# Performance work log

Measured on AMD Instinct MI355X. Metric: run time of the kernel, lower is better.

The kernel has to match this reference:

```python
import jax, jax.numpy as jnp
import numpy as np

ATTN_MASK_VALUE = -1e10
N, D_IN, D_HEAD, D_OUT = 8192, 1024, 128, 1024


def setup_inputs() -> dict:
    key = jax.random.key(0)
    k_x, k_wqkv, k_bqkv, k_wo, k_bo = jax.random.split(key, 5)
    x = jax.random.normal(k_x, (N, D_IN), dtype=jnp.float32)
    # flax Dense default: lecun_normal kernel, zeros bias; use scaled normal for test
    w_qkv = jax.random.normal(k_wqkv, (D_IN, 3 * D_HEAD), dtype=jnp.float32) / np.sqrt(D_IN)
    b_qkv = jnp.zeros((3 * D_HEAD,), dtype=jnp.float32)
    w_out = jax.random.normal(k_wo, (D_HEAD, D_OUT), dtype=jnp.float32) / np.sqrt(D_HEAD)
    b_out = jnp.zeros((D_OUT,), dtype=jnp.float32)
    return {"x": x, "w_qkv": w_qkv, "b_qkv": b_qkv, "w_out": w_out, "b_out": b_out}


def reference(x, w_qkv, b_qkv, w_out, b_out):
    n = x.shape[0]
    scale = D_HEAD ** (-0.5)
    qkv = x @ w_qkv + b_qkv                      # [n, 3*dh]
    q, k, v = jnp.split(qkv, 3, axis=-1)         # each [n, dh]
    sim = jnp.einsum('id,jd->ij', q, k) * scale  # [n, n]
    mask = jnp.triu(jnp.ones((n, n), dtype=bool), 1)
    sim = jnp.where(mask, ATTN_MASK_VALUE, sim)
    attn = jax.nn.softmax(sim, axis=-1)
    out = jnp.einsum('ij,jd->id', attn, v)       # [n, dh]
    return out @ w_out + b_out                   # [n, d_out]
```

## Files before the change

### kernel.cpp

```cpp
#include <hip/hip_runtime.h>
#include <stdint.h>

typedef __attribute__((ext_vector_type(4))) float f32x4;
typedef __attribute__((ext_vector_type(8))) __bf16 bf16x8;

#define MFMA16(a, b, c) __builtin_amdgcn_mfma_f32_16x16x32_bf16(a, b, c, 0, 0, 0)
#define GLOAD16(g, l)                                                              \
  __builtin_amdgcn_global_load_lds(                                                \
      (const __attribute__((address_space(1))) unsigned int*)(g),                  \
      (__attribute__((address_space(3))) unsigned int*)(l), 16, 0, 0)
#define EXP2F(x) __builtin_amdgcn_exp2f(x)

static __device__ __forceinline__ unsigned short f2b(float f) {
  unsigned int u = __float_as_uint(f);
  u += 0x7fff + ((u >> 16) & 1);
  return (unsigned short)(u >> 16);
}
static __device__ __forceinline__ float b2f(unsigned short h) {
  unsigned int u = ((unsigned int)h) << 16;
  return __uint_as_float(u);
}

#define NROWS 8192
#define DIN   1024
#define DH    128
#define DOUT  1024

__global__ void k_convert_w(const float* __restrict__ wqkv, const float* __restrict__ wout,
                            unsigned short* __restrict__ wqkvT, unsigned short* __restrict__ woutT) {
  __shared__ float t[64][65];
  const int bid = blockIdx.x;
  const float* src;
  unsigned short* dst;
  int k0, n0, sstride, dstride;
  if (bid < 96) {
    int kt = bid / 6, nt = bid % 6;
    k0 = kt * 64; n0 = nt * 64;
    src = wqkv; sstride = 384; dst = wqkvT; dstride = 1024;
  } else {
    int b2 = bid - 96;
    int kt = b2 & 1, nt = b2 >> 1;
    k0 = kt * 64; n0 = nt * 64;
    src = wout; sstride = 1024; dst = woutT; dstride = 128;
  }
  const int tid = threadIdx.x;
  const int r = tid >> 4, c4 = (tid & 15) * 4;
#pragma unroll
  for (int j = 0; j < 4; ++j) {
    int rr = r + j * 16;
    float4 v = *reinterpret_cast<const float4*>(src + (size_t)(k0 + rr) * sstride + n0 + c4);
    t[rr][c4 + 0] = v.x; t[rr][c4 + 1] = v.y; t[rr][c4 + 2] = v.z; t[rr][c4 + 3] = v.w;
  }
  __syncthreads();
#pragma unroll
  for (int j = 0; j < 4; ++j) {
    int rn = r + j * 16;
    ushort4 h;
    h.x = f2b(t[c4 + 0][rn]); h.y = f2b(t[c4 + 1][rn]);
    h.z = f2b(t[c4 + 2][rn]); h.w = f2b(t[c4 + 3][rn]);
    *reinterpret_cast<ushort4*>(dst + (size_t)(n0 + rn) * dstride + k0 + c4) = h;
  }
}

__global__ void k_convert_x(const float* __restrict__ x, unsigned short* __restrict__ xb) {
  int i = (blockIdx.x * 256 + threadIdx.x) * 4;
  float4 v = *reinterpret_cast<const float4*>(x + i);
  ushort4 h;
  h.x = f2b(v.x); h.y = f2b(v.y); h.z = f2b(v.z); h.w = f2b(v.w);
  *reinterpret_cast<ushort4*>(xb + i) = h;
}

__launch_bounds__(256, 2)
__global__ void k_qkv_gemm(const unsigned short* __restrict__ xb, const unsigned short* __restrict__ wT,
                           const float* __restrict__ bqkv,
                           unsigned short* __restrict__ Qb, unsigned short* __restrict__ Kb,
                           unsigned short* __restrict__ Vb) {
  const int hb = blockIdx.x;
  const int xcd = hb & 7, jj = hb >> 3;
  const int tau = xcd * 48 + jj;
  const int bn = tau % 6, bm = tau / 6;
  const int tid = threadIdx.x;
  const int lane = tid & 63, w = tid >> 6;
  const int l15 = lane & 15, g = lane >> 4;
  const int wm = (w >> 1) * 64, wn = (w & 1) * 32;
  const int row0 = bm * 128, col0 = bn * 64;

  __shared__ __align__(16) char Ash[2][16384];
  __shared__ __align__(16) char Bsh[2][8192];

  f32x4 acc[4][2] = {};

#define QKV_STAGE(k0, buf)                                                          \
  {                                                                                 \
    _Pragma("unroll")                                                               \
    for (int j2 = 0; j2 < 4; ++j2) {                                                \
      int idx = j2 * 256 + tid;                                                     \
      int r = idx >> 3, gg = idx & 7, sgg = gg ^ (r & 7);                           \
      GLOAD16(xb + (size_t)(row0 + r) * DIN + (k0) + sgg * 8, Ash[buf] + idx * 16); \
    }                                                                               \
    _Pragma("unroll")                                                               \
    for (int j2 = 0; j2 < 2; ++j2) {                                                \
      int idx = j2 * 256 + tid;                                                     \
      int r = idx >> 3, gg = idx & 7, sgg = gg ^ (r & 7);                           \
      GLOAD16(wT + (size_t)(col0 + r) * DIN + (k0) + sgg * 8, Bsh[buf] + idx * 16); \
    }                                                                               \
  }

  QKV_STAGE(0, 0);
  __syncthreads();
  int cur = 0;
  for (int k0 = 0; k0 < DIN; k0 += 64) {
    if (k0 + 64 < DIN) QKV_STAGE(k0 + 64, cur ^ 1);
#pragma unroll
    for (int ksl = 0; ksl < 2; ++ksl) {
      bf16x8 af[4], bfr[2];
#pragma unroll
      for (int i = 0; i < 4; ++i) {
        int r = wm + i * 16 + l15;
        int ba = r * 128 + ksl * 64 + g * 16;
        af[i] = *reinterpret_cast<bf16x8*>(Ash[cur] + (ba ^ ((r & 7) << 4)));
      }
#pragma unroll
      for (int jn = 0; jn < 2; ++jn) {
        int n = wn + jn * 16 + l15;
        int bb = n * 128 + ksl * 64 + g * 16;
        bfr[jn] = *reinterpret_cast<bf16x8*>(Bsh[cur] + (bb ^ ((n & 7) << 4)));
      }
#pragma unroll
      for (int i = 0; i < 4; ++i)
#pragma unroll
        for (int jn = 0; jn < 2; ++jn)
          acc[i][jn] = MFMA16(af[i], bfr[jn], acc[i][jn]);
    }
    __syncthreads();
    cur ^= 1;
  }

  const int which = col0 >> 7;
  const int inner = col0 & 127;
  unsigned short* outb = (which == 0) ? Qb : (which == 1 ? Kb : Vb);
#pragma unroll
  for (int i = 0; i < 4; ++i)
#pragma unroll
    for (int jn = 0; jn < 2; ++jn)
#pragma unroll
      for (int r = 0; r < 4; ++r) {
        int grow = row0 + wm + i * 16 + g * 4 + r;
        int lcol = wn + jn * 16 + l15;
        float vv = acc[i][jn][r] + bqkv[col0 + lcol];
        outb[(size_t)grow * DH + inner + lcol] = f2b(vv);
      }
}

__global__ void k_transpose_v(const unsigned short* __restrict__ V, unsigned short* __restrict__ VT) {
  __shared__ __align__(16) unsigned short t[64 * 128];
  const int b = blockIdx.x;
  const int tid = threadIdx.x;
  const int kv0 = b * 64;
#pragma unroll
  for (int j = 0; j < 4; ++j) {
    int c = j * 256 + tid;
    int r = c >> 4, cc = (c & 15) * 8;
    uint4 v = *reinterpret_cast<const uint4*>(V + (size_t)(kv0 + r) * DH + cc);
    int col = (cc + ((r >> 3) & 7) * 8) & 127;
    *reinterpret_cast<uint4*>(&t[r * 128 + col]) = v;
  }
  __syncthreads();
#pragma unroll
  for (int j = 0; j < 4; ++j) {
    int c = j * 256 + tid;
    int d = c >> 3, kk = (c & 7) * 8;
    unsigned short tmp[8];
#pragma unroll
    for (int e = 0; e < 8; ++e) {
      int r = kk + e;
      int col = (d + ((r >> 3) & 7) * 8) & 127;
      tmp[e] = t[r * 128 + col];
    }
    *reinterpret_cast<uint4*>(VT + (size_t)d * NROWS + kv0 + kk) = *reinterpret_cast<uint4*>(tmp);
  }
}

__launch_bounds__(256, 2)
__global__ void k_flash(const unsigned short* __restrict__ Q, const unsigned short* __restrict__ Kg,
                        const unsigned short* __restrict__ VT,
                        unsigned short* __restrict__ Opart, float* __restrict__ MLpart, int LQ) {
  const int ci = blockIdx.x;
  const int t = (int)(gridDim.y - 1) - (int)blockIdx.y;
  const int Jq = 1 << LQ;
  if (ci * Jq > t) return;
  const int qb = t << 7;
  const int ks = ci * (Jq << 7);
  const int ke = min(ks + (Jq << 7), qb + 128);
  const int nsteps = (ke - ks) >> 6;

  const int a = t >> LQ, b = t & (Jq - 1);
  const int slot = t + ((Jq * a * (a - 1)) >> 1) + a * b + ci;

  const int tid = threadIdx.x;
  const int lane = tid & 63, w = tid >> 6;
  const int l15 = lane & 15, g = lane >> 4;

  __shared__ __align__(16) char Ksh[2][16384];
  __shared__ __align__(16) char Vsh[2][16384];
  __shared__ __align__(16) char Psh[4][4096];

  const int qr0 = qb + w * 16 + l15;
  const int qr1 = qr0 + 64;
  bf16x8 qf0[4], qf1[4];
#pragma unroll
  for (int d = 0; d < 4; ++d) {
    qf0[d] = *reinterpret_cast<const bf16x8*>(Q + (size_t)qr0 * DH + d * 32 + g * 8);
    qf1[d] = *reinterpret_cast<const bf16x8*>(Q + (size_t)qr1 * DH + d * 32 + g * 8);
  }

  f32x4 acco0[8] = {}, acco1[8] = {};
  float m0 = -1e30f, l0 = 0.f, m1 = -1e30f, l1 = 0.f;
  const float c2 = 0.08838834764831843f * 1.4426950408889634f;

#define FL_STAGE(kv0, buf)                                                            \
  {                                                                                   \
    _Pragma("unroll")                                                                 \
    for (int j2 = 0; j2 < 4; ++j2) {                                                  \
      int idx = j2 * 256 + tid;                                                       \
      int r = idx >> 4, gg = idx & 15, sgg = gg ^ (r & 7);                            \
      GLOAD16(Kg + (size_t)((kv0) + r) * DH + sgg * 8, Ksh[buf] + idx * 16);          \
    }                                                                                 \
    _Pragma("unroll")                                                                 \
    for (int j2 = 0; j2 < 4; ++j2) {                                                  \
      int idx = j2 * 256 + tid;                                                       \
      int d = idx >> 3, gg = idx & 7, sgg = gg ^ (d & 7);                             \
      GLOAD16(VT + (size_t)d * NROWS + (kv0) + sgg * 8, Vsh[buf] + idx * 16);         \
    }                                                                                 \
  }

  char* Pw = Psh[w];

  FL_STAGE(ks, 0);
  __syncthreads();
  int cur = 0;

  for (int s = 0; s < nsteps; ++s) {
    const int kv0 = ks + (s << 6);
    if (s + 1 < nsteps) FL_STAGE(kv0 + 64, cur ^ 1);
    const bool act0 = (kv0 < qb + 64);

    f32x4 accs0[4] = {}, accs1[4] = {};
    __builtin_amdgcn_s_setprio(1);
    if (act0) {
#pragma unroll
      for (int jc = 0; jc < 4; ++jc)
#pragma unroll
        for (int d = 0; d < 4; ++d) {
          int r = jc * 16 + l15;
          int byte = r * 256 + d * 64 + g * 16; byte ^= (r & 7) << 4;
          bf16x8 kf = *reinterpret_cast<bf16x8*>(Ksh[cur] + byte);
          accs1[jc] = MFMA16(kf, qf1[d], accs1[jc]);
          accs0[jc] = MFMA16(kf, qf0[d], accs0[jc]);
        }
    } else {
#pragma unroll
      for (int jc = 0; jc < 4; ++jc)
#pragma unroll
        for (int d = 0; d < 4; ++d) {
          int r = jc * 16 + l15;
          int byte = r * 256 + d * 64 + g * 16; byte ^= (r & 7) << 4;
          bf16x8 kf = *reinterpret_cast<bf16x8*>(Ksh[cur] + byte);
          accs1[jc] = MFMA16(kf, qf1[d], accs1[jc]);
        }
    }
    __builtin_amdgcn_s_setprio(0);

#define SOFTMAX_PW(ACCS, ACCO, M, L, QROW, ROWBASE)                                   \
    {                                                                                 \
      float p[4][4];                                                                  \
      float mx = -3e38f;                                                              \
      _Pragma("unroll")                                                               \
      for (int jc = 0; jc < 4; ++jc)                                                  \
        _Pragma("unroll")                                                             \
        for (int r = 0; r < 4; ++r) {                                                 \
          float sv = ACCS[jc][r] * c2;                                                \
          int kk = kv0 + jc * 16 + (g << 2) + r;                                      \
          sv = (kk <= (QROW)) ? sv : -3e38f;                                          \
          p[jc][r] = sv;                                                              \
          mx = fmaxf(mx, sv);                                                         \
        }                                                                             \
      mx = fmaxf(mx, __shfl_xor(mx, 16));                                             \
      mx = fmaxf(mx, __shfl_xor(mx, 32));                                             \
      float mnew = fmaxf(M, mx);                                                      \
      float fac = EXP2F(M - mnew);                                                    \
      float ps = 0.f;                                                                 \
      _Pragma("unroll")                                                               \
      for (int jc = 0; jc < 4; ++jc)                                                  \
        _Pragma("unroll")                                                             \
        for (int r = 0; r < 4; ++r) {                                                 \
          float e = EXP2F(p[jc][r] - mnew);                                           \
          p[jc][r] = e; ps += e;                                                      \
        }                                                                             \
      ps += __shfl_xor(ps, 16);                                                       \
      ps += __shfl_xor(ps, 32);                                                       \
      L = L * fac + ps;                                                               \
      M = mnew;                                                                       \
      _Pragma("unroll")                                                               \
      for (int dc = 0; dc < 8; ++dc)                                                  \
        _Pragma("unroll")                                                             \
        for (int r = 0; r < 4; ++r) ACCO[dc][r] *= fac;                               \
      int rq = (ROWBASE) + l15;                                                       \
      _Pragma("unroll")                                                               \
      for (int jc = 0; jc < 4; ++jc) {                                                \
        ushort4 pb;                                                                   \
        pb.x = f2b(p[jc][0]); pb.y = f2b(p[jc][1]);                                   \
        pb.z = f2b(p[jc][2]); pb.w = f2b(p[jc][3]);                                   \
        int byte = rq * 128 + jc * 32 + g * 8; byte ^= (rq & 7) << 4;                 \
        *reinterpret_cast<ushort4*>(Pw + byte) = pb;                                  \
      }                                                                               \
    }

    if (act0) SOFTMAX_PW(accs0, acco0, m0, l0, qr0, 0);
    SOFTMAX_PW(accs1, acco1, m1, l1, qr1, 16);
    __asm__ volatile("s_waitcnt lgkmcnt(0)" ::: "memory");
    __builtin_amdgcn_sched_barrier(0);

    bf16x8 pf1[2];
#pragma unroll
    for (int ks2 = 0; ks2 < 2; ++ks2) {
      int rq = 16 + l15;
      int byte = rq * 128 + ks2 * 64 + g * 16; byte ^= (rq & 7) << 4;
      pf1[ks2] = *reinterpret_cast<bf16x8*>(Pw + byte);
    }
    __builtin_amdgcn_s_setprio(1);
    if (act0) {
      bf16x8 pf0[2];
#pragma unroll
      for (int ks2 = 0; ks2 < 2; ++ks2) {
        int byte = l15 * 128 + ks2 * 64 + g * 16; byte ^= (l15 & 7) << 4;
        pf0[ks2] = *reinterpret_cast<bf16x8*>(Pw + byte);
      }
#pragma unroll
      for (int dc = 0; dc < 8; ++dc) {
        int vr = dc * 16 + l15;
        int b0 = vr * 128 + g * 16; b0 ^= (vr & 7) << 4;
        bf16x8 vf0 = *reinterpret_cast<bf16x8*>(Vsh[cur] + b0);
        bf16x8 vf1 = *reinterpret_cast<bf16x8*>(Vsh[cur] + (b0 ^ 64));
        acco1[dc] = MFMA16(vf0, pf1[0], acco1[dc]);
        acco1[dc] = MFMA16(vf1, pf1[1], acco1[dc]);
        acco0[dc] = MFMA16(vf0, pf0[0], acco0[dc]);
        acco0[dc] = MFMA16(vf1, pf0[1], acco0[dc]);
      }
    } else {
#pragma unroll
      for (int dc = 0; dc < 8; ++dc) {
        int vr = dc * 16 + l15;
        int b0 = vr * 128 + g * 16; b0 ^= (vr & 7) << 4;
        bf16x8 vf0 = *reinterpret_cast<bf16x8*>(Vsh[cur] + b0);
        bf16x8 vf1 = *reinterpret_cast<bf16x8*>(Vsh[cur] + (b0 ^ 64));
        acco1[dc] = MFMA16(vf0, pf1[0], acco1[dc]);
        acco1[dc] = MFMA16(vf1, pf1[1], acco1[dc]);
      }
    }
    __builtin_amdgcn_s_setprio(0);
    __syncthreads();
    cur ^= 1;
  }

  const size_t r0 = (size_t)slot * 128 + w * 16 + l15;
  const size_t r1 = r0 + 64;
#pragma unroll
  for (int dc = 0; dc < 8; ++dc) {
    ushort4 o0, o1;
    o0.x = f2b(acco0[dc][0]); o0.y = f2b(acco0[dc][1]);
    o0.z = f2b(acco0[dc][2]); o0.w = f2b(acco0[dc][3]);
    o1.x = f2b(acco1[dc][0]); o1.y = f2b(acco1[dc][1]);
    o1.z = f2b(acco1[dc][2]); o1.w = f2b(acco1[dc][3]);
    *reinterpret_cast<ushort4*>(Opart + r0 * DH + dc * 16 + (g << 2)) = o0;
    *reinterpret_cast<ushort4*>(Opart + r1 * DH + dc * 16 + (g << 2)) = o1;
  }
  if (g == 0) {
    MLpart[r0 * 2 + 0] = m0;
    MLpart[r0 * 2 + 1] = l0;
    MLpart[r1 * 2 + 0] = m1;
    MLpart[r1 * 2 + 1] = l1;
  }
}

__global__ void k_merge(const unsigned short* __restrict__ Opart, const float* __restrict__ MLpart,
                        unsigned short* __restrict__ O, int LQ) {
  int tg = blockIdx.x * 256 + threadIdx.x;
  int row = tg >> 5, d4 = (tg & 31) * 4;
  int t = row >> 7;
  int Jq = 1 << LQ;
  int a = t >> LQ, b = t & (Jq - 1);
  int base = t + ((Jq * a * (a - 1)) >> 1) + a * b;
  int nc = a + 1;
  int rowin = row & 127;
  float M = -3e38f;
  for (int i = 0; i < nc; ++i) M = fmaxf(M, MLpart[((size_t)(base + i) * 128 + rowin) * 2]);
  float L = 0.f;
  f32x4 acc = {};
  for (int i = 0; i < nc; ++i) {
    size_t sr = (size_t)(base + i) * 128 + rowin;
    float mi = MLpart[sr * 2];
    float li = MLpart[sr * 2 + 1];
    float wg = EXP2F(mi - M);
    L += li * wg;
    ushort4 o = *reinterpret_cast<const ushort4*>(Opart + sr * DH + d4);
    acc[0] += wg * b2f(o.x); acc[1] += wg * b2f(o.y);
    acc[2] += wg * b2f(o.z); acc[3] += wg * b2f(o.w);
  }
  float inv = 1.f / L;
  ushort4 hv;
  hv.x = f2b(acc[0] * inv); hv.y = f2b(acc[1] * inv);
  hv.z = f2b(acc[2] * inv); hv.w = f2b(acc[3] * inv);
  *reinterpret_cast<ushort4*>(O + (size_t)row * DH + d4) = hv;
}

__launch_bounds__(256, 2)
__global__ void k_out_gemm(const unsigned short* __restrict__ O, const unsigned short* __restrict__ wT,
                           const float* __restrict__ bout, float* __restrict__ out) {
  const int hb = blockIdx.x;
  const int xcd = hb & 7, jj = hb >> 3;
  const int tau = xcd * 64 + jj;
  const int bn = tau & 7, bm = tau >> 3;
  const int tid = threadIdx.x;
  const int lane = tid & 63, w = tid >> 6;
  const int l15 = lane & 15, g = lane >> 4;
  const int wm = (w >> 1) * 64, wn = (w & 1) * 64;
  const int row0 = bm * 128, col0 = bn * 128;

  __shared__ __align__(16) char Ash[2][16384];
  __shared__ __align__(16) char Bsh[2][16384];

  f32x4 acc[4][4] = {};

#define OUT_STAGE(k0, buf)                                                          \
  {                                                                                 \
    _Pragma("unroll")                                                               \
    for (int j2 = 0; j2 < 4; ++j2) {                                                \
      int idx = j2 * 256 + tid;                                                     \
      int r = idx >> 3, gg = idx & 7, sgg = gg ^ (r & 7);                           \
      GLOAD16(O + (size_t)(row0 + r) * DH + (k0) + sgg * 8, Ash[buf] + idx * 16);   \
      GLOAD16(wT + (size_t)(col0 + r) * DH + (k0) + sgg * 8, Bsh[buf] + idx * 16);  \
    }                                                                               \
  }

  OUT_STAGE(0, 0);
  __syncthreads();
  int cur = 0;
  for (int k0 = 0; k0 < DH; k0 += 64) {
    if (k0 + 64 < DH) OUT_STAGE(k0 + 64, cur ^ 1);
#pragma unroll
    for (int ksl = 0; ksl < 2; ++ksl) {
      bf16x8 af[4], bfr[4];
#pragma unroll
      for (int i = 0; i < 4; ++i) {
        int r = wm + i * 16 + l15;
        int ba = r * 128 + ksl * 64 + g * 16;
        af[i] = *reinterpret_cast<bf16x8*>(Ash[cur] + (ba ^ ((r & 7) << 4)));
        int n = wn + i * 16 + l15;
        int bb = n * 128 + ksl * 64 + g * 16;
        bfr[i] = *reinterpret_cast<bf16x8*>(Bsh[cur] + (bb ^ ((n & 7) << 4)));
      }
#pragma unroll
      for (int i = 0; i < 4; ++i)
#pragma unroll
        for (int jn = 0; jn < 4; ++jn)
          acc[i][jn] = MFMA16(af[i], bfr[jn], acc[i][jn]);
    }
    __syncthreads();
    cur ^= 1;
  }

#pragma unroll
  for (int i = 0; i < 4; ++i)
#pragma unroll
    for (int jn = 0; jn < 4; ++jn)
#pragma unroll
      for (int r = 0; r < 4; ++r) {
        int grow = row0 + wm + i * 16 + g * 4 + r;
        int gcol = col0 + wn + jn * 16 + l15;
        out[(size_t)grow * DOUT + gcol] = acc[i][jn][r] + bout[gcol];
      }
}

extern "C" void kernel_launch(void* const* d_in, const int* in_sizes, int n_in,
                              void* d_out, int out_size, void* d_ws, size_t ws_size,
                              hipStream_t stream) {
  const float* x    = (const float*)d_in[0];
  const float* wqkv = (const float*)d_in[1];
  const float* bqkv = (const float*)d_in[2];
  const float* wout = (const float*)d_in[3];
  const float* bout = (const float*)d_in[4];
  float* out = (float*)d_out;

  size_t fixed = 786432 + 262144 + (size_t)NROWS * DIN * 2 + (size_t)5 * NROWS * DH * 2;
  int LQ = 2;
  size_t slots = 0;
  for (; LQ <= 6; ++LQ) {
    int Jq = 1 << LQ, A = 64 / Jq;
    slots = (size_t)Jq * A * (A + 1) / 2;
    size_t need = fixed + slots * ((size_t)128 * DH * 2 + 128 * 8);
    if (need <= ws_size || LQ == 6) break;
  }

  char* ws = (char*)d_ws;
  size_t off = 0;
  unsigned short* wqkvT = (unsigned short*)(ws + off); off += (size_t)384 * 1024 * 2;
  unsigned short* woutT = (unsigned short*)(ws + off); off += (size_t)1024 * 128 * 2;
  unsigned short* xb  = (unsigned short*)(ws + off); off += (size_t)NROWS * DIN * 2;
  unsigned short* Qb  = (unsigned short*)(ws + off); off += (size_t)NROWS * DH * 2;
  unsigned short* Kb  = (unsigned short*)(ws + off); off += (size_t)NROWS * DH * 2;
  unsigned short* Vb  = (unsigned short*)(ws + off); off += (size_t)NROWS * DH * 2;
  unsigned short* VTb = (unsigned short*)(ws + off); off += (size_t)NROWS * DH * 2;
  unsigned short* Ob  = (unsigned short*)(ws + off); off += (size_t)NROWS * DH * 2;
  unsigned short* Opart = (unsigned short*)(ws + off); off += slots * (size_t)128 * DH * 2;
  float* MLpart = (float*)(ws + off); off += slots * (size_t)128 * 8;

  k_convert_w<<<128, 256, 0, stream>>>(wqkv, wout, wqkvT, woutT);
  k_convert_x<<<(NROWS * DIN) / 1024, 256, 0, stream>>>(x, xb);
  k_qkv_gemm<<<384, 256, 0, stream>>>(xb, wqkvT, bqkv, Qb, Kb, Vb);
  k_transpose_v<<<128, 256, 0, stream>>>(Vb, VTb);
  k_flash<<<dim3(64 >> LQ, 64), 256, 0, stream>>>(Qb, Kb, VTb, Opart, MLpart, LQ);
  k_merge<<<(NROWS * 32) / 256, 256, 0, stream>>>(Opart, MLpart, Ob, LQ);
  k_out_gemm<<<512, 256, 0, stream>>>(Ob, woutT, bout, out);
}
```

Measured before the change: 115.5 us.

## Merge convert kernels, add lazy softmax rescale, use packed bf16 conversion

Merges the x and weight fp32-to-bf16 conversion kernels into one launch, saving one kernel launch. In the flash softmax, it rescales the running max and accumulator only when a wave's new max exceeds the old one by more than 8 (log2 domain), skipping most rescale multiplies. Manual round-to-nearest bf16 packing is replaced with the hardware v_cvt_pk_bf16_f32 instruction in the flash, output and merge stores. An explicit lgkmcnt wait and sched barrier after the softmax P-write is removed. The lazy-rescale threshold lets exponentials reach up to 2^8 before renormalisation, and dropping the LDS wait may create a race unless a later barrier covers it.

```diff
diff --git a/kernel.cpp b/kernel.cpp
--- a/kernel.cpp
+++ b/kernel.cpp
@@ -20,30 +20,46 @@
   unsigned int u = ((unsigned int)h) << 16;
   return __uint_as_float(u);
 }
+static __device__ __forceinline__ unsigned int cvt_pk_bf16(float a, float b) {
+  unsigned int r;
+  asm("v_cvt_pk_bf16_f32 %0, %1, %2" : "=v"(r) : "v"(a), "v"(b));
+  return r;
+}
 
 #define NROWS 8192
 #define DIN   1024
 #define DH    128
 #define DOUT  1024
 
-__global__ void k_convert_w(const float* __restrict__ wqkv, const float* __restrict__ wout,
-                            unsigned short* __restrict__ wqkvT, unsigned short* __restrict__ woutT) {
+__global__ void k_convert(const float* __restrict__ x, const float* __restrict__ wqkv,
+                          const float* __restrict__ wout,
+                          unsigned short* __restrict__ xb,
+                          unsigned short* __restrict__ wqkvT, unsigned short* __restrict__ woutT) {
+  const int bid = blockIdx.x;
+  const int tid = threadIdx.x;
+  if (bid < 8192) {
+    int i = (bid * 256 + tid) * 4;
+    float4 v = *reinterpret_cast<const float4*>(x + i);
+    ushort4 h;
+    h.x = f2b(v.x); h.y = f2b(v.y); h.z = f2b(v.z); h.w = f2b(v.w);
+    *reinterpret_cast<ushort4*>(xb + i) = h;
+    return;
+  }
   __shared__ float t[64][65];
-  const int bid = blockIdx.x;
+  const int wb = bid - 8192;
   const float* src;
   unsigned short* dst;
   int k0, n0, sstride, dstride;
-  if (bid < 96) {
-    int kt = bid / 6, nt = bid % 6;
+  if (wb < 96) {
+    int kt = wb / 6, nt = wb % 6;
     k0 = kt * 64; n0 = nt * 64;
     src = wqkv; sstride = 384; dst = wqkvT; dstride = 1024;
   } else {
-    int b2 = bid - 96;
+    int b2 = wb - 96;
     int kt = b2 & 1, nt = b2 >> 1;
     k0 = kt * 64; n0 = nt * 64;
     src = wout; sstride = 1024; dst = woutT; dstride = 128;
   }
-  const int tid = threadIdx.x;
   const int r = tid >> 4, c4 = (tid & 15) * 4;
 #pragma unroll
   for (int j = 0; j < 4; ++j) {
@@ -60,14 +76,6 @@
     h.z = f2b(t[c4 + 2][rn]); h.w = f2b(t[c4 + 3][rn]);
     *reinterpret_cast<ushort4*>(dst + (size_t)(n0 + rn) * dstride + k0 + c4) = h;
   }
-}
-
-__global__ void k_convert_x(const float* __restrict__ x, unsigned short* __restrict__ xb) {
-  int i = (blockIdx.x * 256 + threadIdx.x) * 4;
-  float4 v = *reinterpret_cast<const float4*>(x + i);
-  ushort4 h;
-  h.x = f2b(v.x); h.y = f2b(v.y); h.z = f2b(v.z); h.w = f2b(v.w);
-  *reinterpret_cast<ushort4*>(xb + i) = h;
 }
 
 __launch_bounds__(256, 2)
@@ -287,39 +295,40 @@
         }                                                                             \
       mx = fmaxf(mx, __shfl_xor(mx, 16));                                             \
       mx = fmaxf(mx, __shfl_xor(mx, 32));                                             \
-      float mnew = fmaxf(M, mx);                                                      \
-      float fac = EXP2F(M - mnew);                                                    \
+      if (!__all(mx <= M + 8.f)) {             \
+        float mnew = fmaxf(M, mx);                                                    \
+        float fac = EXP2F(M - mnew);                                                  \
+        L *= fac;                                                                     \
+        M = mnew;                                                                     \
+        _Pragma("unroll")                                                             \
+        for (int dc = 0; dc < 8; ++dc)                                                \
+          _Pragma("unroll")                                                           \
+          for (int r = 0; r < 4; ++r) ACCO[dc][r] *= fac;                             \
+      }                                                                               \
       float ps = 0.f;                                                                 \
       _Pragma("unroll")                                                               \
       for (int jc = 0; jc < 4; ++jc)                                                  \
         _Pragma("unroll")                                                             \
         for (int r = 0; r < 4; ++r) {                                                 \
-          float e = EXP2F(p[jc][r] - mnew);                                           \
+          float e = EXP2F(p[jc][r] - M);                                              \
           p[jc][r] = e; ps += e;                                                      \
         }                                                                             \
       ps += __shfl_xor(ps, 16);                                                       \
       ps += __shfl_xor(ps, 32);                                                       \
-      L = L * fac + ps;                                                               \
-      M = mnew;                                                                       \
-      _Pragma("unroll")                                                               \
-      for (int dc = 0; dc < 8; ++dc)                                                  \
-        _Pragma("unroll")                                                             \
-        for (int r = 0; r < 4; ++r) ACCO[dc][r] *= fac;                               \
+      L += ps;                                                                        \
       int rq = (ROWBASE) + l15;                                                       \
       _Pragma("unroll")                                                               \
       for (int jc = 0; jc < 4; ++jc) {                                                \
-        ushort4 pb;                                                                   \
-        pb.x = f2b(p[jc][0]); pb.y = f2b(p[jc][1]);                                   \
-        pb.z = f2b(p[jc][2]); pb.w = f2b(p[jc][3]);                                   \
+        uint2 pb;                                                                     \
+        pb.x = cvt_pk_bf16(p[jc][0], p[jc][1]);                                       \
+        pb.y = cvt_pk_bf16(p[jc][2], p[jc][3]);                                       \
         int byte = rq * 128 + jc * 32 + g * 8; byte ^= (rq & 7) << 4;                 \
-        *reinterpret_cast<ushort4*>(Pw + byte) = pb;                                  \
+        *reinterpret_cast<uint2*>(Pw + byte) = pb;                                    \
       }                                                                               \
     }
 
     if (act0) SOFTMAX_PW(accs0, acco0, m0, l0, qr0, 0);
     SOFTMAX_PW(accs1, acco1, m1, l1, qr1, 16);
-    __asm__ volatile("s_waitcnt lgkmcnt(0)" ::: "memory");
-    __builtin_amdgcn_sched_barrier(0);
 
     bf16x8 pf1[2];
 #pragma unroll
@@ -367,13 +376,13 @@
   const size_t r1 = r0 + 64;
 #pragma unroll
   for (int dc = 0; dc < 8; ++dc) {
-    ushort4 o0, o1;
-    o0.x = f2b(acco0[dc][0]); o0.y = f2b(acco0[dc][1]);
-    o0.z = f2b(acco0[dc][2]); o0.w = f2b(acco0[dc][3]);
-    o1.x = f2b(acco1[dc][0]); o1.y = f2b(acco1[dc][1]);
-    o1.z = f2b(acco1[dc][2]); o1.w = f2b(acco1[dc][3]);
-    *reinterpret_cast<ushort4*>(Opart + r0 * DH + dc * 16 + (g << 2)) = o0;
-    *reinterpret_cast<ushort4*>(Opart + r1 * DH + dc * 16 + (g << 2)) = o1;
+    uint2 o0, o1;
+    o0.x = cvt_pk_bf16(acco0[dc][0], acco0[dc][1]);
+    o0.y = cvt_pk_bf16(acco0[dc][2], acco0[dc][3]);
+    o1.x = cvt_pk_bf16(acco1[dc][0], acco1[dc][1]);
+    o1.y = cvt_pk_bf16(acco1[dc][2], acco1[dc][3]);
+    *reinterpret_cast<uint2*>(Opart + r0 * DH + dc * 16 + (g << 2)) = o0;
+    *reinterpret_cast<uint2*>(Opart + r1 * DH + dc * 16 + (g << 2)) = o1;
   }
   if (g == 0) {
     MLpart[r0 * 2 + 0] = m0;
@@ -408,10 +417,10 @@
     acc[2] += wg * b2f(o.z); acc[3] += wg * b2f(o.w);
   }
   float inv = 1.f / L;
-  ushort4 hv;
-  hv.x = f2b(acc[0] * inv); hv.y = f2b(acc[1] * inv);
-  hv.z = f2b(acc[2] * inv); hv.w = f2b(acc[3] * inv);
-  *reinterpret_cast<ushort4*>(O + (size_t)row * DH + d4) = hv;
+  uint2 hv;
+  hv.x = cvt_pk_bf16(acc[0] * inv, acc[1] * inv);
+  hv.y = cvt_pk_bf16(acc[2] * inv, acc[3] * inv);
+  *reinterpret_cast<uint2*>(O + (size_t)row * DH + d4) = hv;
 }
 
 __launch_bounds__(256, 2)
@@ -515,8 +524,7 @@
   unsigned short* Opart = (unsigned short*)(ws + off); off += slots * (size_t)128 * DH * 2;
   float* MLpart = (float*)(ws + off); off += slots * (size_t)128 * 8;
 
-  k_convert_w<<<128, 256, 0, stream>>>(wqkv, wout, wqkvT, woutT);
-  k_convert_x<<<(NROWS * DIN) / 1024, 256, 0, stream>>>(x, xb);
+  k_convert<<<8320, 256, 0, stream>>>(x, wqkv, wout, xb, wqkvT, woutT);
   k_qkv_gemm<<<384, 256, 0, stream>>>(xb, wqkvT, bqkv, Qb, Kb, Vb);
   k_transpose_v<<<128, 256, 0, stream>>>(Vb, VTb);
   k_flash<<<dim3(64 >> LQ, 64), 256, 0, stream>>>(Qb, Kb, VTb, Opart, MLpart, LQ);
```

New measurement: 110.8 us. -4.1%, faster.
